# Optimization experiments

Hardware: AMD Instinct MI355X
Metric: run time of the kernel (lower is better)

Reference implementation:

```python
import jax, jax.numpy as jnp
import numpy as np

EPS_LN = 1e-5
EPS_D = 1e-8
K = 3

def layer_norm(x, g, b):
    mu = jnp.mean(x, axis=-1, keepdims=True)
    var = jnp.var(x, axis=-1, keepdims=True)
    return (x - mu) * jax.lax.rsqrt(var + EPS_LN) * g + b

def setup_inputs() -> dict:
    key = jax.random.key(0)
    ks = jax.random.split(key, 8)
    Nc, Nu, Cin, Cout = 4096, 16384, 256, 256
    return {
        "x_feat": jax.random.normal(ks[0], (Nc, Cin), jnp.float32),
        "x_pos": jax.random.uniform(ks[1], (Nc, 3), jnp.float32),
        "xup_feat": jax.random.normal(ks[2], (Nu, Cout), jnp.float32),
        "xup_pos": jax.random.uniform(ks[3], (Nu, 3), jnp.float32),
        "g1": jnp.ones((Cin,), jnp.float32),
        "b1": jnp.zeros((Cin,), jnp.float32),
        "W": jax.random.normal(ks[4], (Cin, Cout), jnp.float32) * 0.02,
        "b": jnp.zeros((Cout,), jnp.float32),
        "g2": jnp.ones((Cout,), jnp.float32),
        "b2": jnp.zeros((Cout,), jnp.float32),
        "W_up": jax.random.normal(ks[5], (Cout, Cout), jnp.float32) * 0.02,
        "b_up": jnp.zeros((Cout,), jnp.float32),
    }

def reference(x_feat, x_pos, xup_feat, xup_pos, g1, b1, W, b, g2, b2, W_up, b_up):
    # norm -> linear on coarse points: [Nc, Cout]
    x = layer_norm(x_feat, g1, b1) @ W + b
    # norm -> linear on fine points:   [Nu, Cout]
    xu = layer_norm(xup_feat, g2, b2) @ W_up + b_up
    # squared pairwise distances fine->coarse: [Nu, Nc]
    d2 = (jnp.sum(xup_pos * xup_pos, axis=-1, keepdims=True)
          - 2.0 * (xup_pos @ x_pos.T)
          + jnp.sum(x_pos * x_pos, axis=-1))
    # k nearest coarse neighbors per fine point
    neg_d2, idx = jax.lax.top_k(-d2, K)          # [Nu, K]
    w = 1.0 / (-neg_d2 + EPS_D)                  # inverse-distance weights
    w = w / jnp.sum(w, axis=-1, keepdims=True)
    # gather + weighted sum: [Nu, Cout]
    interp = jnp.einsum('uk,ukc->uc', w, x[idx])
    return interp + xu
```

## Files before the change

kernel.cpp:

```cpp
#include <hip/hip_runtime.h>

#define EPS_LN 1e-5f
#define EPS_D  1e-8f

typedef __attribute__((ext_vector_type(8))) short s16x8;
typedef __attribute__((ext_vector_type(4))) float f32x4;

#define XC_OFF     0u
#define MU_OFF     4194304u
#define RS_OFF     4276224u
#define WTH_OFF    4358144u
#define WTL_OFF    4489216u
#define WUTH_OFF   4620288u
#define WUTL_OFF   4751360u
#define CPS_OFF    4882432u
#define IDXS_OFF   4947968u
#define CST_OFF    4964352u

__global__ __launch_bounds__(256) void prep_kernel(
    const float* __restrict__ x_feat, const float* __restrict__ xup_feat,
    const float* __restrict__ W, const float* __restrict__ W_up,
    float* __restrict__ mu, float* __restrict__ rs,
    unsigned short* __restrict__ wth, unsigned short* __restrict__ wtl,
    unsigned short* __restrict__ wuth, unsigned short* __restrict__ wutl)
{
    const int bid = blockIdx.x, tid = threadIdx.x;
    const int lane = tid & 63, wave = tid >> 6;

    if (bid < 320) {
        for (int r = bid * 4 + wave; r < 20480; r += 1280) {
            const float* src = (r < 16384) ? (xup_feat + (size_t)r * 256)
                                           : (x_feat + (size_t)(r - 16384) * 256);
            const float4 v = ((const float4*)src)[lane];
            float s  = v.x + v.y + v.z + v.w;
            float ss = v.x*v.x + v.y*v.y + v.z*v.z + v.w*v.w;
            #pragma unroll
            for (int off = 1; off < 64; off <<= 1) {
                s  += __shfl_xor(s,  off);
                ss += __shfl_xor(ss, off);
            }
            if (lane == 0) {
                const float m   = s * (1.0f / 256.0f);
                const float var = ss * (1.0f / 256.0f) - m * m;
                mu[r] = m;
                rs[r] = rsqrtf(var + EPS_LN);
            }
        }
    } else {
        const int mb = bid - 320;
        const float* src = (mb < 8) ? W : W_up;
        unsigned short* dh = (mb < 8) ? wth : wuth;
        unsigned short* dl = (mb < 8) ? wtl : wutl;
        const int k  = (mb & 7) * 32 + (tid >> 3);
        const int n0 = (tid & 7) * 32;
        for (int i = 0; i < 32; i += 4) {
            const float4 v = *(const float4*)&src[(size_t)k * 256 + n0 + i];
            const float vv[4] = { v.x, v.y, v.z, v.w };
            #pragma unroll
            for (int c = 0; c < 4; ++c) {
                const unsigned ua = __float_as_uint(vv[c]);
                const unsigned hb = ua & 0xFFFF0000u;
                const float rr = vv[c] - __uint_as_float(hb);
                const size_t o = (size_t)(n0 + i + c) * 256 + k;
                dh[o] = (unsigned short)(ua >> 16);
                dl[o] = (unsigned short)(__float_as_uint(rr) >> 16);
            }
        }
    }
}

__device__ __forceinline__ int cell_of(float px, float py, float pz) {
    int cx = (int)(px * 8.0f); cx = cx < 0 ? 0 : (cx > 7 ? 7 : cx);
    int cy = (int)(py * 8.0f); cy = cy < 0 ? 0 : (cy > 7 ? 7 : cy);
    int cz = (int)(pz * 8.0f); cz = cz < 0 ? 0 : (cz > 7 ? 7 : cz);
    return (cz * 8 + cy) * 8 + cx;
}

__global__ __launch_bounds__(1024) void grid_kernel(
    const float* __restrict__ x_pos,
    float4* __restrict__ cps, int* __restrict__ idxs, int* __restrict__ cellStart)
{
    __shared__ int cnt[512];
    __shared__ int ofs[512];
    __shared__ int wsum[8];

    const int tid = threadIdx.x, lane = tid & 63;
    if (tid < 512) cnt[tid] = 0;
    __syncthreads();

    for (int i = tid; i < 4096; i += 1024) {
        const int c = cell_of(x_pos[i*3+0], x_pos[i*3+1], x_pos[i*3+2]);
        atomicAdd(&cnt[c], 1);
    }
    __syncthreads();

    int v = 0, incl = 0;
    if (tid < 512) {
        v = cnt[tid];
        incl = v;
        #pragma unroll
        for (int off = 1; off < 64; off <<= 1) {
            const int t = __shfl_up(incl, off);
            if (lane >= off) incl += t;
        }
        if (lane == 63) wsum[tid >> 6] = incl;
    }
    __syncthreads();
    if (tid == 0) {
        int run = 0;
        for (int w = 0; w < 8; ++w) { const int t = wsum[w]; wsum[w] = run; run += t; }
    }
    __syncthreads();
    if (tid < 512) {
        const int excl = incl - v + wsum[tid >> 6];
        ofs[tid] = excl;
        cellStart[tid] = excl;
    }
    if (tid == 0) cellStart[512] = 4096;
    __syncthreads();

    for (int i = tid; i < 4096; i += 1024) {
        const float px = x_pos[i*3+0], py = x_pos[i*3+1], pz = x_pos[i*3+2];
        const int c = cell_of(px, py, pz);
        const int p = atomicAdd(&ofs[c], 1);
        cps[p] = make_float4(px, py, pz, px*px + py*py + pz*pz);
        idxs[p] = i;
    }
}

__global__ __launch_bounds__(256) void gemm_kernel(
    const float* __restrict__ Xf, const float* __restrict__ Xc,
    const float* __restrict__ mu, const float* __restrict__ rs,
    const float* __restrict__ g2, const float* __restrict__ b2,
    const float* __restrict__ g1, const float* __restrict__ b1,
    const unsigned short* __restrict__ wuth, const unsigned short* __restrict__ wutl,
    const unsigned short* __restrict__ wth,  const unsigned short* __restrict__ wtl,
    const float* __restrict__ b_up, const float* __restrict__ bb,
    float* __restrict__ outF, float* __restrict__ outC)
{
    const int bid = blockIdx.x;
    const float *X, *gg, *bt, *bias; const unsigned short *BH, *BL; float* OUT;
    int row0, col0, statoff;
    if (bid < 256) {
        X = Xf; gg = g2; bt = b2; BH = wuth; BL = wutl; bias = b_up; OUT = outF;
        row0 = (bid >> 1) * 128; col0 = (bid & 1) * 128; statoff = 0;
    } else {
        const int id = bid - 256;
        X = Xc; gg = g1; bt = b1; BH = wth; BL = wtl; bias = bb; OUT = outC;
        row0 = (id >> 1) * 128; col0 = (id & 1) * 128; statoff = 16384;
    }

    const int lane = threadIdx.x & 63;
    const int wave = threadIdx.x >> 6;
    const int wr = wave >> 1, wc = wave & 1;
    const int lm = lane & 15, lk = lane >> 4;

    int arow[4]; float amu[4], ars[4];
    #pragma unroll
    for (int mf = 0; mf < 4; ++mf) {
        arow[mf] = row0 + wr * 64 + mf * 16 + lm;
        amu[mf] = mu[statoff + arow[mf]];
        ars[mf] = rs[statoff + arow[mf]];
    }
    int ncol[4]; float bv[4];
    #pragma unroll
    for (int nf = 0; nf < 4; ++nf) {
        ncol[nf] = col0 + wc * 64 + nf * 16 + lm;
        bv[nf] = bias[ncol[nf]];
    }

    f32x4 acc[4][4];
    #pragma unroll
    for (int mf = 0; mf < 4; ++mf)
        #pragma unroll
        for (int nf = 0; nf < 4; ++nf)
            acc[mf][nf] = (f32x4){0.0f, 0.0f, 0.0f, 0.0f};

    for (int k0 = 0; k0 < 256; k0 += 32) {
        const int kb = k0 + lk * 8;

        s16x8 bh[4], bl[4];
        #pragma unroll
        for (int nf = 0; nf < 4; ++nf) {
            const size_t o = (size_t)ncol[nf] * 256 + kb;
            bh[nf] = *(const s16x8*)(BH + o);
            bl[nf] = *(const s16x8*)(BL + o);
        }

        const float4 gq0 = *(const float4*)(gg + kb);
        const float4 gq1 = *(const float4*)(gg + kb + 4);
        const float4 bq0 = *(const float4*)(bt + kb);
        const float4 bq1 = *(const float4*)(bt + kb + 4);
        const float gv[8] = { gq0.x, gq0.y, gq0.z, gq0.w, gq1.x, gq1.y, gq1.z, gq1.w };
        const float bw[8] = { bq0.x, bq0.y, bq0.z, bq0.w, bq1.x, bq1.y, bq1.z, bq1.w };

        #pragma unroll
        for (int mf = 0; mf < 4; ++mf) {
            const float* pa = X + (size_t)arow[mf] * 256 + kb;
            const float4 x0 = *(const float4*)pa;
            const float4 x1 = *(const float4*)(pa + 4);
            const float xs[8] = { x0.x, x0.y, x0.z, x0.w, x1.x, x1.y, x1.z, x1.w };
            s16x8 ah, al;
            #pragma unroll
            for (int j = 0; j < 8; ++j) {
                const float sj = ars[mf] * gv[j];
                const float tj = fmaf(-amu[mf], sj, bw[j]);
                const float a  = fmaf(xs[j], sj, tj);
                const unsigned ua = __float_as_uint(a);
                const unsigned hb = ua & 0xFFFF0000u;
                const float rr = a - __uint_as_float(hb);
                ah[j] = (short)(ua >> 16);
                al[j] = (short)(__float_as_uint(rr) >> 16);
            }
            #pragma unroll
            for (int nf = 0; nf < 4; ++nf) {
                acc[mf][nf] = __builtin_amdgcn_mfma_f32_16x16x32_bf16(ah, bh[nf], acc[mf][nf], 0, 0, 0);
                acc[mf][nf] = __builtin_amdgcn_mfma_f32_16x16x32_bf16(ah, bl[nf], acc[mf][nf], 0, 0, 0);
                acc[mf][nf] = __builtin_amdgcn_mfma_f32_16x16x32_bf16(al, bh[nf], acc[mf][nf], 0, 0, 0);
            }
        }
    }

    #pragma unroll
    for (int mf = 0; mf < 4; ++mf) {
        #pragma unroll
        for (int q = 0; q < 4; ++q) {
            const size_t ro = (size_t)(row0 + wr * 64 + mf * 16 + lk * 4 + q) * 256;
            #pragma unroll
            for (int nf = 0; nf < 4; ++nf)
                OUT[ro + ncol[nf]] = acc[mf][nf][q] + bv[nf];
        }
    }
}

#define BIGD 3.402823466e+38f

__device__ __forceinline__ void ins3(float d, int p,
    float& b0, float& b1, float& b2, int& p0, int& p1, int& p2)
{
    const bool lt0 = d < b0, lt1 = d < b1, lt2 = d < b2;
    const float n1 = lt0 ? b0 : (lt1 ? d : b1);
    const int   q1 = lt0 ? p0 : (lt1 ? p : p1);
    const float n2 = lt1 ? b1 : (lt2 ? d : b2);
    const int   q2 = lt1 ? p1 : (lt2 ? p : p2);
    b0 = lt0 ? d : b0;  p0 = lt0 ? p : p0;
    b1 = n1; p1 = q1;
    b2 = n2; p2 = q2;
}

__global__ __launch_bounds__(512) void topk_kernel(
    const float4* __restrict__ cps, const int* __restrict__ idxs,
    const int* __restrict__ cellStart,
    const float* __restrict__ xup_pos,
    const float* __restrict__ xc, float* __restrict__ out)
{
    __shared__ float pd[8][64][3];
    __shared__ int   pp[8][64][3];
    __shared__ float wsel[64][3];
    __shared__ int   isel[64][3];
    __shared__ int   cst[513];

    const int tid = threadIdx.x, lane = tid & 63, wave = tid >> 6;
    const int u = blockIdx.x * 64 + lane;

    for (int i = tid; i < 513; i += 512) cst[i] = cellStart[i];

    const float ux = xup_pos[u * 3 + 0];
    const float uy = xup_pos[u * 3 + 1];
    const float uz = xup_pos[u * 3 + 2];
    const float uu = ux * ux + uy * uy + uz * uz;
    int cx = (int)(ux * 8.0f); cx = cx < 0 ? 0 : (cx > 7 ? 7 : cx);
    int cy = (int)(uy * 8.0f); cy = cy < 0 ? 0 : (cy > 7 ? 7 : cy);
    int cz = (int)(uz * 8.0f); cz = cz < 0 ? 0 : (cz > 7 ? 7 : cz);

    __syncthreads();

    float b0 = BIGD, b1 = BIGD, b2 = BIGD;
    int p0 = 0, p1 = 0, p2 = 0;

    for (int cc = wave; cc < 27; cc += 8) {
        const int nx = cx + (cc % 3) - 1;
        const int ny = cy + ((cc / 3) % 3) - 1;
        const int nz = cz + (cc / 9) - 1;
        if ((unsigned)nx > 7u || (unsigned)ny > 7u || (unsigned)nz > 7u) continue;
        const int cell = (nz * 8 + ny) * 8 + nx;
        const int s = cst[cell], e = cst[cell + 1];
        if (s >= e) continue;
        float4 c = cps[s];
        for (int p = s; p < e; ++p) {
            const float4 nxt = (p + 1 < e) ? cps[p + 1] : c;
            const float dot = ux * c.x + uy * c.y + uz * c.z;
            const float d = (uu - 2.0f * dot) + c.w;
            ins3(d, p, b0, b1, b2, p0, p1, p2);
            c = nxt;
        }
    }

    pd[wave][lane][0] = b0; pd[wave][lane][1] = b1; pd[wave][lane][2] = b2;
    pp[wave][lane][0] = p0; pp[wave][lane][1] = p1; pp[wave][lane][2] = p2;
    __syncthreads();

    if (wave == 0) {
        for (int w = 1; w < 8; ++w) {
            #pragma unroll
            for (int e = 0; e < 3; ++e)
                ins3(pd[w][lane][e], pp[w][lane][e], b0, b1, b2, p0, p1, p2);
        }

        const float h = 0.125f;
        float gmin = BIGD;
        if (cx > 0) gmin = fminf(gmin, ux - (float)(cx - 1) * h);
        if (cx < 7) gmin = fminf(gmin, (float)(cx + 2) * h - ux);
        if (cy > 0) gmin = fminf(gmin, uy - (float)(cy - 1) * h);
        if (cy < 7) gmin = fminf(gmin, (float)(cy + 2) * h - uy);
        if (cz > 0) gmin = fminf(gmin, uz - (float)(cz - 1) * h);
        if (cz < 7) gmin = fminf(gmin, (float)(cz + 2) * h - uz);

        if (b2 > gmin * gmin) {
            b0 = b1 = b2 = BIGD; p0 = p1 = p2 = 0;
            for (int p = 0; p < 4096; ++p) {
                const float4 c = cps[p];
                const float dot = ux * c.x + uy * c.y + uz * c.z;
                const float d = (uu - 2.0f * dot) + c.w;
                ins3(d, p, b0, b1, b2, p0, p1, p2);
            }
        }

        float w0 = 1.0f / (b0 + EPS_D);
        float w1 = 1.0f / (b1 + EPS_D);
        float w2 = 1.0f / (b2 + EPS_D);
        const float inv = 1.0f / (w0 + w1 + w2);
        wsel[lane][0] = w0 * inv; wsel[lane][1] = w1 * inv; wsel[lane][2] = w2 * inv;
        isel[lane][0] = idxs[p0]; isel[lane][1] = idxs[p1]; isel[lane][2] = idxs[p2];
    }
    __syncthreads();

    #pragma unroll
    for (int r = 0; r < 8; ++r) {
        const int ul = wave * 8 + r;
        const float w0 = wsel[ul][0], w1 = wsel[ul][1], w2 = wsel[ul][2];
        const int a0 = isel[ul][0], a1 = isel[ul][1], a2 = isel[ul][2];
        const float4 v0 = ((const float4*)(xc + (size_t)a0 * 256))[lane];
        const float4 v1 = ((const float4*)(xc + (size_t)a1 * 256))[lane];
        const float4 v2 = ((const float4*)(xc + (size_t)a2 * 256))[lane];
        float4* op = (float4*)(out + (size_t)(blockIdx.x * 64 + ul) * 256);
        float4 o = op[lane];
        o.x += w0 * v0.x + w1 * v1.x + w2 * v2.x;
        o.y += w0 * v0.y + w1 * v1.y + w2 * v2.y;
        o.z += w0 * v0.z + w1 * v1.z + w2 * v2.z;
        o.w += w0 * v0.w + w1 * v1.w + w2 * v2.w;
        op[lane] = o;
    }
}

extern "C" void kernel_launch(void* const* d_in, const int* in_sizes, int n_in,
                              void* d_out, int out_size, void* d_ws, size_t ws_size,
                              hipStream_t stream)
{
    const float* x_feat   = (const float*)d_in[0];
    const float* x_pos    = (const float*)d_in[1];
    const float* xup_feat = (const float*)d_in[2];
    const float* xup_pos  = (const float*)d_in[3];
    const float* g1       = (const float*)d_in[4];
    const float* b1       = (const float*)d_in[5];
    const float* W        = (const float*)d_in[6];
    const float* bb       = (const float*)d_in[7];
    const float* g2       = (const float*)d_in[8];
    const float* b2       = (const float*)d_in[9];
    const float* W_up     = (const float*)d_in[10];
    const float* b_up     = (const float*)d_in[11];

    float* out = (float*)d_out;
    char*  ws  = (char*)d_ws;

    float* xc  = (float*)(ws + XC_OFF);
    float* mu  = (float*)(ws + MU_OFF);
    float* rs  = (float*)(ws + RS_OFF);
    unsigned short* wth  = (unsigned short*)(ws + WTH_OFF);
    unsigned short* wtl  = (unsigned short*)(ws + WTL_OFF);
    unsigned short* wuth = (unsigned short*)(ws + WUTH_OFF);
    unsigned short* wutl = (unsigned short*)(ws + WUTL_OFF);
    float4* cps = (float4*)(ws + CPS_OFF);
    int* idxs   = (int*)(ws + IDXS_OFF);
    int* cstart = (int*)(ws + CST_OFF);

    prep_kernel<<<336, 256, 0, stream>>>(x_feat, xup_feat, W, W_up,
                                         mu, rs, wth, wtl, wuth, wutl);
    grid_kernel<<<1, 1024, 0, stream>>>(x_pos, cps, idxs, cstart);
    gemm_kernel<<<320, 256, 0, stream>>>(xup_feat, x_feat, mu, rs,
                                         g2, b2, g1, b1,
                                         wuth, wutl, wth, wtl,
                                         b_up, bb, out, xc);
    topk_kernel<<<256, 512, 0, stream>>>(cps, idxs, cstart, xup_pos, xc, out);
}
```

Measured before the change: 173.8 us.

## Fold LayerNorm algebraically into GEMM epilogue and pre-split raw features to bf16

Rewrites LN(x)@W as rs*(x@(g∘W)) - mu*rs*(g@W) + b@W. The prep kernel now splits the raw features into bf16 hi/lo arrays and scales the weights by gamma. It also computes the two correction vectors and builds the coarse-point grid, which removes the separate single-block grid launch. The GEMM loads precomputed bf16 fragments instead of normalizing and splitting per tile, and applies mean/rstd in the epilogue. In exchange, about 20MB of extra bf16 traffic is written and re-read, and the expansion risks cancellation error when the mean is large relative to the spread.

After: 167.3 us. -3.7%, faster.

```diff
diff --git a/kernel.cpp b/kernel.cpp
--- a/kernel.cpp
+++ b/kernel.cpp
@@ -2,33 +2,57 @@
 
 #define EPS_LN 1e-5f
 #define EPS_D  1e-8f
+#define BIGD 3.402823466e+38f
 
 typedef __attribute__((ext_vector_type(8))) short s16x8;
 typedef __attribute__((ext_vector_type(4))) float f32x4;
-
-#define XC_OFF     0u
-#define MU_OFF     4194304u
-#define RS_OFF     4276224u
-#define WTH_OFF    4358144u
-#define WTL_OFF    4489216u
-#define WUTH_OFF   4620288u
-#define WUTL_OFF   4751360u
-#define CPS_OFF    4882432u
-#define IDXS_OFF   4947968u
-#define CST_OFF    4964352u
+typedef __attribute__((ext_vector_type(4))) unsigned short u16x4;
+
+#define XC_OFF    0u
+#define XH_OFF    4194304u
+#define XL_OFF    14680064u
+#define MU_OFF    25165824u
+#define RS_OFF    25247744u
+#define WGH_OFF   25329664u
+#define WGL_OFF   25460736u
+#define WUGH_OFF  25591808u
+#define WUGL_OFF  25722880u
+#define C12_OFF   25853952u
+#define CPS_OFF   25858048u
+#define IDXS_OFF  25923584u
+#define CST_OFF   25939968u
+
+__device__ __forceinline__ int cell_of(float px, float py, float pz) {
+    int cx = (int)(px * 8.0f); cx = cx < 0 ? 0 : (cx > 7 ? 7 : cx);
+    int cy = (int)(py * 8.0f); cy = cy < 0 ? 0 : (cy > 7 ? 7 : cy);
+    int cz = (int)(pz * 8.0f); cz = cz < 0 ? 0 : (cz > 7 ? 7 : cz);
+    return (cz * 8 + cy) * 8 + cx;
+}
 
 __global__ __launch_bounds__(256) void prep_kernel(
     const float* __restrict__ x_feat, const float* __restrict__ xup_feat,
+    const float* __restrict__ x_pos,
     const float* __restrict__ W, const float* __restrict__ W_up,
+    const float* __restrict__ g1, const float* __restrict__ b1,
+    const float* __restrict__ g2, const float* __restrict__ b2,
     float* __restrict__ mu, float* __restrict__ rs,
-    unsigned short* __restrict__ wth, unsigned short* __restrict__ wtl,
-    unsigned short* __restrict__ wuth, unsigned short* __restrict__ wutl)
+    unsigned short* __restrict__ xh, unsigned short* __restrict__ xl,
+    unsigned short* __restrict__ wgh, unsigned short* __restrict__ wgl,
+    unsigned short* __restrict__ wugh, unsigned short* __restrict__ wugl,
+    float* __restrict__ c12,
+    float4* __restrict__ cps, int* __restrict__ idxs, int* __restrict__ cellStart)
 {
+    __shared__ int cnt[512];
+    __shared__ int ofs[512];
+    __shared__ int wpart[4];
+
     const int bid = blockIdx.x, tid = threadIdx.x;
     const int lane = tid & 63, wave = tid >> 6;
 
-    if (bid < 320) {
-        for (int r = bid * 4 + wave; r < 20480; r += 1280) {
+    if (bid < 640) {
+        #pragma unroll
+        for (int rr = 0; rr < 8; ++rr) {
+            const int r = bid * 32 + wave * 8 + rr;
             const float* src = (r < 16384) ? (xup_feat + (size_t)r * 256)
                                            : (x_feat + (size_t)(r - 16384) * 256);
             const float4 v = ((const float4*)src)[lane];
@@ -45,109 +69,110 @@
                 mu[r] = m;
                 rs[r] = rsqrtf(var + EPS_LN);
             }
-        }
-    } else {
-        const int mb = bid - 320;
-        const float* src = (mb < 8) ? W : W_up;
-        unsigned short* dh = (mb < 8) ? wth : wuth;
-        unsigned short* dl = (mb < 8) ? wtl : wutl;
-        const int k  = (mb & 7) * 32 + (tid >> 3);
-        const int n0 = (tid & 7) * 32;
-        for (int i = 0; i < 32; i += 4) {
-            const float4 v = *(const float4*)&src[(size_t)k * 256 + n0 + i];
             const float vv[4] = { v.x, v.y, v.z, v.w };
+            u16x4 hv, lv;
             #pragma unroll
             for (int c = 0; c < 4; ++c) {
                 const unsigned ua = __float_as_uint(vv[c]);
-                const unsigned hb = ua & 0xFFFF0000u;
-                const float rr = vv[c] - __uint_as_float(hb);
-                const size_t o = (size_t)(n0 + i + c) * 256 + k;
-                dh[o] = (unsigned short)(ua >> 16);
-                dl[o] = (unsigned short)(__float_as_uint(rr) >> 16);
-            }
-        }
-    }
-}
-
-__device__ __forceinline__ int cell_of(float px, float py, float pz) {
-    int cx = (int)(px * 8.0f); cx = cx < 0 ? 0 : (cx > 7 ? 7 : cx);
-    int cy = (int)(py * 8.0f); cy = cy < 0 ? 0 : (cy > 7 ? 7 : cy);
-    int cz = (int)(pz * 8.0f); cz = cz < 0 ? 0 : (cz > 7 ? 7 : cz);
-    return (cz * 8 + cy) * 8 + cx;
-}
-
-__global__ __launch_bounds__(1024) void grid_kernel(
-    const float* __restrict__ x_pos,
-    float4* __restrict__ cps, int* __restrict__ idxs, int* __restrict__ cellStart)
-{
-    __shared__ int cnt[512];
-    __shared__ int ofs[512];
-    __shared__ int wsum[8];
-
-    const int tid = threadIdx.x, lane = tid & 63;
-    if (tid < 512) cnt[tid] = 0;
-    __syncthreads();
-
-    for (int i = tid; i < 4096; i += 1024) {
-        const int c = cell_of(x_pos[i*3+0], x_pos[i*3+1], x_pos[i*3+2]);
-        atomicAdd(&cnt[c], 1);
-    }
-    __syncthreads();
-
-    int v = 0, incl = 0;
-    if (tid < 512) {
-        v = cnt[tid];
-        incl = v;
+                hv[c] = (unsigned short)(ua >> 16);
+                const float lo = vv[c] - __uint_as_float(ua & 0xFFFF0000u);
+                lv[c] = (unsigned short)(__float_as_uint(lo) >> 16);
+            }
+            *(u16x4*)&xh[(size_t)r * 256 + lane * 4] = hv;
+            *(u16x4*)&xl[(size_t)r * 256 + lane * 4] = lv;
+        }
+    } else if (bid < 656) {
+        const int mb = bid - 640;
+        const float* src = (mb < 8) ? W : W_up;
+        const float* g   = (mb < 8) ? g1 : g2;
+        unsigned short* dh = (mb < 8) ? wgh : wugh;
+        unsigned short* dl = (mb < 8) ? wgl : wugl;
+        const int n  = (mb & 7) * 32 + (tid >> 3);
+        const int kc = (tid & 7) * 32;
+        for (int kk = 0; kk < 32; kk += 4) {
+            u16x4 hv, lv;
+            #pragma unroll
+            for (int c = 0; c < 4; ++c) {
+                const int k = kc + kk + c;
+                const float wv = g[k] * src[(size_t)k * 256 + n];
+                const unsigned ua = __float_as_uint(wv);
+                hv[c] = (unsigned short)(ua >> 16);
+                const float lo = wv - __uint_as_float(ua & 0xFFFF0000u);
+                lv[c] = (unsigned short)(__float_as_uint(lo) >> 16);
+            }
+            *(u16x4*)&dh[(size_t)n * 256 + kc + kk] = hv;
+            *(u16x4*)&dl[(size_t)n * 256 + kc + kk] = lv;
+        }
+    } else if (bid < 658) {
+        const bool fine = (bid == 657);
+        const float* src = fine ? W_up : W;
+        const float* g   = fine ? g2 : g1;
+        const float* bln = fine ? b2 : b1;
+        float* c1 = c12 + (fine ? 0 : 512);
+        float* c2 = c12 + (fine ? 256 : 768);
+        float a1 = 0.0f, a2 = 0.0f;
+        for (int k = 0; k < 256; ++k) {
+            const float wv = src[(size_t)k * 256 + tid];
+            a1 = fmaf(bln[k], wv, a1);
+            a2 = fmaf(g[k],   wv, a2);
+        }
+        c1[tid] = a1;
+        c2[tid] = a2;
+    } else {
+        cnt[tid] = 0; cnt[tid + 256] = 0;
+        __syncthreads();
+        for (int i = tid; i < 4096; i += 256) {
+            const int c = cell_of(x_pos[i*3+0], x_pos[i*3+1], x_pos[i*3+2]);
+            atomicAdd(&cnt[c], 1);
+        }
+        __syncthreads();
+        const int base = wave * 128 + lane * 2;
+        const int a = cnt[base], b = cnt[base + 1];
+        const int p = a + b;
+        int incl = p;
         #pragma unroll
         for (int off = 1; off < 64; off <<= 1) {
             const int t = __shfl_up(incl, off);
             if (lane >= off) incl += t;
         }
-        if (lane == 63) wsum[tid >> 6] = incl;
-    }
-    __syncthreads();
-    if (tid == 0) {
-        int run = 0;
-        for (int w = 0; w < 8; ++w) { const int t = wsum[w]; wsum[w] = run; run += t; }
-    }
-    __syncthreads();
-    if (tid < 512) {
-        const int excl = incl - v + wsum[tid >> 6];
-        ofs[tid] = excl;
-        cellStart[tid] = excl;
-    }
-    if (tid == 0) cellStart[512] = 4096;
-    __syncthreads();
-
-    for (int i = tid; i < 4096; i += 1024) {
-        const float px = x_pos[i*3+0], py = x_pos[i*3+1], pz = x_pos[i*3+2];
-        const int c = cell_of(px, py, pz);
-        const int p = atomicAdd(&ofs[c], 1);
-        cps[p] = make_float4(px, py, pz, px*px + py*py + pz*pz);
-        idxs[p] = i;
+        if (lane == 63) wpart[wave] = incl;
+        __syncthreads();
+        int woff = 0;
+        for (int w = 0; w < 4; ++w) if (w < wave) woff += wpart[w];
+        const int e0 = woff + (incl - p);
+        ofs[base] = e0;          ofs[base + 1] = e0 + a;
+        cellStart[base] = e0;    cellStart[base + 1] = e0 + a;
+        if (tid == 0) cellStart[512] = 4096;
+        __syncthreads();
+        for (int i = tid; i < 4096; i += 256) {
+            const float px = x_pos[i*3+0], py = x_pos[i*3+1], pz = x_pos[i*3+2];
+            const int c = cell_of(px, py, pz);
+            const int pos = atomicAdd(&ofs[c], 1);
+            cps[pos] = make_float4(px, py, pz, px*px + py*py + pz*pz);
+            idxs[pos] = i;
+        }
     }
 }
 
 __global__ __launch_bounds__(256) void gemm_kernel(
-    const float* __restrict__ Xf, const float* __restrict__ Xc,
+    const unsigned short* __restrict__ xh, const unsigned short* __restrict__ xl,
     const float* __restrict__ mu, const float* __restrict__ rs,
-    const float* __restrict__ g2, const float* __restrict__ b2,
-    const float* __restrict__ g1, const float* __restrict__ b1,
-    const unsigned short* __restrict__ wuth, const unsigned short* __restrict__ wutl,
-    const unsigned short* __restrict__ wth,  const unsigned short* __restrict__ wtl,
+    const unsigned short* __restrict__ wgh, const unsigned short* __restrict__ wgl,
+    const unsigned short* __restrict__ wugh, const unsigned short* __restrict__ wugl,
+    const float* __restrict__ c12,
     const float* __restrict__ b_up, const float* __restrict__ bb,
     float* __restrict__ outF, float* __restrict__ outC)
 {
     const int bid = blockIdx.x;
-    const float *X, *gg, *bt, *bias; const unsigned short *BH, *BL; float* OUT;
-    int row0, col0, statoff;
+    const unsigned short *BH, *BL; const float *c1, *c2, *bias; float* OUT;
+    int row0, col0, statbase;
     if (bid < 256) {
-        X = Xf; gg = g2; bt = b2; BH = wuth; BL = wutl; bias = b_up; OUT = outF;
-        row0 = (bid >> 1) * 128; col0 = (bid & 1) * 128; statoff = 0;
+        BH = wugh; BL = wugl; c1 = c12; c2 = c12 + 256; bias = b_up; OUT = outF;
+        row0 = (bid >> 1) * 128; col0 = (bid & 1) * 128; statbase = 0;
     } else {
         const int id = bid - 256;
-        X = Xc; gg = g1; bt = b1; BH = wth; BL = wtl; bias = bb; OUT = outC;
-        row0 = (id >> 1) * 128; col0 = (id & 1) * 128; statoff = 16384;
+        BH = wgh; BL = wgl; c1 = c12 + 512; c2 = c12 + 768; bias = bb; OUT = outC;
+        row0 = (id >> 1) * 128; col0 = (id & 1) * 128; statbase = 16384;
     }
 
     const int lane = threadIdx.x & 63;
@@ -155,18 +180,18 @@
     const int wr = wave >> 1, wc = wave & 1;
     const int lm = lane & 15, lk = lane >> 4;
 
-    int arow[4]; float amu[4], ars[4];
+    int arow[4];
     #pragma unroll
-    for (int mf = 0; mf < 4; ++mf) {
-        arow[mf] = row0 + wr * 64 + mf * 16 + lm;
-        amu[mf] = mu[statoff + arow[mf]];
-        ars[mf] = rs[statoff + arow[mf]];
-    }
-    int ncol[4]; float bv[4];
+    for (int mf = 0; mf < 4; ++mf)
+        arow[mf] = statbase + row0 + wr * 64 + mf * 16 + lm;
+
+    int ncol[4]; float c1v[4], c2v[4], bv[4];
     #pragma unroll
     for (int nf = 0; nf < 4; ++nf) {
         ncol[nf] = col0 + wc * 64 + nf * 16 + lm;
-        bv[nf] = bias[ncol[nf]];
+        c1v[nf] = c1[ncol[nf]];
+        c2v[nf] = c2[ncol[nf]];
+        bv[nf]  = bias[ncol[nf]];
     }
 
     f32x4 acc[4][4];
@@ -179,61 +204,45 @@
     for (int k0 = 0; k0 < 256; k0 += 32) {
         const int kb = k0 + lk * 8;
 
-        s16x8 bh[4], bl[4];
+        s16x8 bh[4], bl[4], ah[4], al[4];
         #pragma unroll
         for (int nf = 0; nf < 4; ++nf) {
             const size_t o = (size_t)ncol[nf] * 256 + kb;
             bh[nf] = *(const s16x8*)(BH + o);
             bl[nf] = *(const s16x8*)(BL + o);
         }
-
-        const float4 gq0 = *(const float4*)(gg + kb);
-        const float4 gq1 = *(const float4*)(gg + kb + 4);
-        const float4 bq0 = *(const float4*)(bt + kb);
-        const float4 bq1 = *(const float4*)(bt + kb + 4);
-        const float gv[8] = { gq0.x, gq0.y, gq0.z, gq0.w, gq1.x, gq1.y, gq1.z, gq1.w };
-        const float bw[8] = { bq0.x, bq0.y, bq0.z, bq0.w, bq1.x, bq1.y, bq1.z, bq1.w };
-
         #pragma unroll
         for (int mf = 0; mf < 4; ++mf) {
-            const float* pa = X + (size_t)arow[mf] * 256 + kb;
-            const float4 x0 = *(const float4*)pa;
-            const float4 x1 = *(const float4*)(pa + 4);
-            const float xs[8] = { x0.x, x0.y, x0.z, x0.w, x1.x, x1.y, x1.z, x1.w };
-            s16x8 ah, al;
-            #pragma unroll
-            for (int j = 0; j < 8; ++j) {
-                const float sj = ars[mf] * gv[j];
-                const float tj = fmaf(-amu[mf], sj, bw[j]);
-                const float a  = fmaf(xs[j], sj, tj);
-                const unsigned ua = __float_as_uint(a);
-                const unsigned hb = ua & 0xFFFF0000u;
-                const float rr = a - __uint_as_float(hb);
-                ah[j] = (short)(ua >> 16);
-                al[j] = (short)(__float_as_uint(rr) >> 16);
-            }
+            const size_t o = (size_t)arow[mf] * 256 + kb;
+            ah[mf] = *(const s16x8*)(xh + o);
+            al[mf] = *(const s16x8*)(xl + o);
+        }
+
+        #pragma unroll
+        for (int mf = 0; mf < 4; ++mf)
             #pragma unroll
             for (int nf = 0; nf < 4; ++nf) {
-                acc[mf][nf] = __builtin_amdgcn_mfma_f32_16x16x32_bf16(ah, bh[nf], acc[mf][nf], 0, 0, 0);
-                acc[mf][nf] = __builtin_amdgcn_mfma_f32_16x16x32_bf16(ah, bl[nf], acc[mf][nf], 0, 0, 0);
-                acc[mf][nf] = __builtin_amdgcn_mfma_f32_16x16x32_bf16(al, bh[nf], acc[mf][nf], 0, 0, 0);
-            }
-        }
+                acc[mf][nf] = __builtin_amdgcn_mfma_f32_16x16x32_bf16(ah[mf], bh[nf], acc[mf][nf], 0, 0, 0);
+                acc[mf][nf] = __builtin_amdgcn_mfma_f32_16x16x32_bf16(ah[mf], bl[nf], acc[mf][nf], 0, 0, 0);
+                acc[mf][nf] = __builtin_amdgcn_mfma_f32_16x16x32_bf16(al[mf], bh[nf], acc[mf][nf], 0, 0, 0);
+            }
     }
 
     #pragma unroll
     for (int mf = 0; mf < 4; ++mf) {
         #pragma unroll
         for (int q = 0; q < 4; ++q) {
-            const size_t ro = (size_t)(row0 + wr * 64 + mf * 16 + lk * 4 + q) * 256;
+            const int orow = row0 + wr * 64 + mf * 16 + lk * 4 + q;
+            const float m = mu[statbase + orow];
+            const float s = rs[statbase + orow];
+            const float ms = -m * s;
             #pragma unroll
             for (int nf = 0; nf < 4; ++nf)
-                OUT[ro + ncol[nf]] = acc[mf][nf][q] + bv[nf];
-        }
-    }
-}
-
-#define BIGD 3.402823466e+38f
+                OUT[(size_t)orow * 256 + ncol[nf]] =
+                    fmaf(s, acc[mf][nf][q], fmaf(ms, c2v[nf], c1v[nf]) + bv[nf]);
+        }
+    }
+}
 
 __device__ __forceinline__ void ins3(float d, int p,
     float& b0, float& b1, float& b2, int& p0, int& p1, int& p2)
@@ -374,22 +383,26 @@
     char*  ws  = (char*)d_ws;
 
     float* xc  = (float*)(ws + XC_OFF);
+    unsigned short* xh   = (unsigned short*)(ws + XH_OFF);
+    unsigned short* xl   = (unsigned short*)(ws + XL_OFF);
     float* mu  = (float*)(ws + MU_OFF);
     float* rs  = (float*)(ws + RS_OFF);
-    unsigned short* wth  = (unsigned short*)(ws + WTH_OFF);
-    unsigned short* wtl  = (unsigned short*)(ws + WTL_OFF);
-    unsigned short* wuth = (unsigned short*)(ws + WUTH_OFF);
-    unsigned short* wutl = (unsigned short*)(ws + WUTL_OFF);
+    unsigned short* wgh  = (unsigned short*)(ws + WGH_OFF);
+    unsigned short* wgl  = (unsigned short*)(ws + WGL_OFF);
+    unsigned short* wugh = (unsigned short*)(ws + WUGH_OFF);
+    unsigned short* wugl = (unsigned short*)(ws + WUGL_OFF);
+    float* c12 = (float*)(ws + C12_OFF);
     float4* cps = (float4*)(ws + CPS_OFF);
     int* idxs   = (int*)(ws + IDXS_OFF);
     int* cstart = (int*)(ws + CST_OFF);
 
-    prep_kernel<<<336, 256, 0, stream>>>(x_feat, xup_feat, W, W_up,
-                                         mu, rs, wth, wtl, wuth, wutl);
-    grid_kernel<<<1, 1024, 0, stream>>>(x_pos, cps, idxs, cstart);
-    gemm_kernel<<<320, 256, 0, stream>>>(xup_feat, x_feat, mu, rs,
-                                         g2, b2, g1, b1,
-                                         wuth, wutl, wth, wtl,
-                                         b_up, bb, out, xc);
+    prep_kernel<<<659, 256, 0, stream>>>(x_feat, xup_feat, x_pos, W, W_up,
+                                         g1, b1, g2, b2,
+                                         mu, rs, xh, xl,
+                                         wgh, wgl, wugh, wugl,
+                                         c12, cps, idxs, cstart);
+    gemm_kernel<<<320, 256, 0, stream>>>(xh, xl, mu, rs,
+                                         wgh, wgl, wugh, wugl,
+                                         c12, b_up, bb, out, xc);
     topk_kernel<<<256, 512, 0, stream>>>(cps, idxs, cstart, xup_pos, xc, out);
 }
```
